# Kernel tuning notes

Hardware: AMD Instinct MI355X
Metric: run time of the kernel (lower is better)

The kernel has to match this reference:

```python
import jax, jax.numpy as jnp
import numpy as np

B = 32
M = 3
MAG_DIM = 20
STD = 0.28
INV = float(1.0 / (np.sqrt(2.0) * STD))
NORM = float(1.0 / (np.sqrt(2.0 * np.pi) * STD))


def _lrelu(x):
    return jax.nn.leaky_relu(x, 0.01)


def _conv(x, w, b):
    y = jax.lax.conv_general_dilated(x, w, (2, 2), 'VALID',
                                     dimension_numbers=('NCHW', 'OIHW', 'NCHW'))
    return _lrelu(y + b[None, :, None, None])


def _combos(x):
    # x: [N, c, d] -> [N, c, c, 2d], pairs[n, i, j] = concat(x[n, i], x[n, j])
    # (matches torch getCombinations: tensorB = expand-over-i, tensorA = expand-over-j)
    N, c, d = x.shape
    left = jnp.broadcast_to(x[:, :, None, :], (N, c, c, d))
    right = jnp.broadcast_to(x[:, None, :, :], (N, c, c, d))
    return jnp.concatenate([left, right], axis=-1)


def _forward(batch, conv_w1, conv_b1, conv_w2, conv_b2, conv_w3, conv_b3, conv_w4, conv_b4,
             post_w, post_b, g_w1, g_b1, g_w2, g_b2, g_w3, g_b3, g_w4, g_b4,
             h_w1, h_b1, h_w2, h_b2, h_w3, h_b3, f_w1, f_b1, f_w2, f_b2, ff_w, ff_b):
    bsz = batch.shape[0]
    x = batch.reshape(bsz * 16, 1, 80, 80)
    # magnitude encoding (computed under no_grad in the original)
    mag = jnp.linspace(-1.0, 1.0, MAG_DIM).astype(batch.dtype)  # [20]
    t = jnp.tanh(x * (2.0 / 255.0) - 1.0)                        # [N,1,80,80]
    enc = NORM * jnp.exp(-(((t + mag[None, :, None, None]) * INV) ** 2))  # [N,20,80,80]
    enc = jax.lax.stop_gradient(enc)
    y = _conv(enc, conv_w1, conv_b1)   # [N,32,39,39]
    y = _conv(y, conv_w2, conv_b2)     # [N,32,19,19]
    y = _conv(y, conv_w3, conv_b3)     # [N,32,9,9]
    y = _conv(y, conv_w4, conv_b4)     # [N,32,4,4]
    obj = y.reshape(bsz * 16, 512) @ post_w + post_b             # [N,247]
    panel = obj.reshape(bsz, 16, 247)
    given, options = panel[:, :8], panel[:, 8:]
    giv = jnp.broadcast_to(given[:, None], (bsz, 8, 8, 247))
    ctx = jnp.concatenate([giv, options[:, :, None, :]], axis=2)  # [B,8,9,247]
    tags = jnp.broadcast_to(jnp.eye(9, dtype=batch.dtype), (bsz * 8, 9, 9))
    objects = jnp.concatenate([ctx.reshape(bsz * 8, 9, 247), tags], axis=-1)  # [B*8,9,256]

    z = _combos(objects).reshape(-1, 512)  # [B*8*81, 512]
    z = _lrelu(z @ g_w1 + g_b1)
    z = _lrelu(z @ g_w2 + g_b2)
    z = _lrelu(z @ g_w3 + g_b3)
    z = _lrelu(z @ g_w4 + g_b4)
    sum_j = z.reshape(bsz * 8, 9, 9, 256).sum(axis=2)  # [B*8,9,256]
    for i in range(h_w1.shape[0]):
        p = _combos(sum_j).reshape(-1, 512)
        z = _lrelu(p @ h_w1[i] + h_b1[i])
        z = _lrelu(z @ h_w2[i] + h_b2[i])
        z = _lrelu(z @ h_w3[i] + h_b3[i])
        sum_j = z.reshape(bsz * 8, 9, 9, 256).sum(axis=2)
    h_sum = sum_j.sum(axis=1)                          # [B*8,256]
    z = _lrelu(h_sum @ f_w1 + f_b1)
    z = _lrelu(z @ f_w2 + f_b2)
    result = z @ ff_w + ff_b                           # [B*8,1]
    answer = result.reshape(bsz, 8)
    loss = jnp.mean(h_sum ** 2) + jnp.mean(result ** 2)
    return answer, loss


def setup_inputs():
    key = jax.random.key(0)
    ks = iter(jax.random.split(key, 40))

    def U(shape, fan_in):
        s = 1.0 / np.sqrt(fan_in)
        return jax.random.uniform(next(ks), shape, jnp.float32, -s, s)

    inp = {
        'batch': jax.random.uniform(next(ks), (B, 16, 80, 80), jnp.float32, 0.0, 255.0),
        'conv_w1': U((32, MAG_DIM, 3, 3), MAG_DIM * 9), 'conv_b1': U((32,), MAG_DIM * 9),
        'conv_w2': U((32, 32, 3, 3), 288), 'conv_b2': U((32,), 288),
        'conv_w3': U((32, 32, 3, 3), 288), 'conv_b3': U((32,), 288),
        'conv_w4': U((32, 32, 3, 3), 288), 'conv_b4': U((32,), 288),
        'post_w': U((512, 247), 512), 'post_b': U((247,), 512),
        'g_w1': U((512, 512), 512), 'g_b1': U((512,), 512),
        'g_w2': U((512, 512), 512), 'g_b2': U((512,), 512),
        'g_w3': U((512, 512), 512), 'g_b3': U((512,), 512),
        'g_w4': U((512, 256), 512), 'g_b4': U((256,), 512),
        'h_w1': U((M, 512, 256), 512), 'h_b1': U((M, 256), 512),
        'h_w2': U((M, 256, 256), 256), 'h_b2': U((M, 256), 256),
        'h_w3': U((M, 256, 256), 256), 'h_b3': U((M, 256), 256),
        'f_w1': U((256, 256), 256), 'f_b1': U((256,), 256),
        'f_w2': U((256, 256), 256), 'f_b2': U((256,), 256),
        'ff_w': U((256, 1), 256), 'ff_b': U((1,), 256),
    }
    return inp


def reference(batch, conv_w1, conv_b1, conv_w2, conv_b2, conv_w3, conv_b3, conv_w4, conv_b4,
              post_w, post_b, g_w1, g_b1, g_w2, g_b2, g_w3, g_b3, g_w4, g_b4,
              h_w1, h_b1, h_w2, h_b2, h_w3, h_b3, f_w1, f_b1, f_w2, f_b2, ff_w, ff_b):
    return _forward(batch, conv_w1, conv_b1, conv_w2, conv_b2, conv_w3, conv_b3, conv_w4, conv_b4,
                    post_w, post_b, g_w1, g_b1, g_w2, g_b2, g_w3, g_b3, g_w4, g_b4,
                    h_w1, h_b1, h_w2, h_b2, h_w3, h_b3, f_w1, f_b1, f_w2, f_b2, ff_w, ff_b)
```

## Files before the change

### kernel.cpp

```cpp
#include <hip/hip_runtime.h>
#include <hip/hip_bf16.h>
#include <math.h>

static __device__ __forceinline__ float lrelu(float v){ return v > 0.0f ? v : 0.01f*v; }

static __device__ __forceinline__ unsigned short f2bf(float f){
  unsigned int u = __float_as_uint(f);
  unsigned int r = (u + 0x7fffu + ((u >> 16) & 1u)) >> 16;
  return (unsigned short)r;
}
static __device__ __forceinline__ float bf2f(unsigned short u){
  return __uint_as_float(((unsigned int)u) << 16);
}
static __device__ __forceinline__ unsigned int pack_bf2(float lo, float hi){
  __hip_bfloat162 bb = __float22bfloat162_rn(make_float2(lo, hi));
  return *reinterpret_cast<unsigned int*>(&bb);
}

#define ENC_NORM 1.4247939f
#define GC_C     6.3775511f
#define GC_2CD   1.3426423f
#define GC_CD2   0.070665395f
#define GC_S1    0.86820227f

typedef __attribute__((ext_vector_type(4))) float f32x4;
typedef __attribute__((ext_vector_type(8))) short bf16x8;

__global__ __launch_bounds__(256) void k_prep(
    const float* __restrict__ g_w1, const float* __restrict__ g_w2,
    const float* __restrict__ g_w3, const float* __restrict__ g_w4,
    const float* __restrict__ h_w1, const float* __restrict__ h_w2,
    const float* __restrict__ h_w3, const float* __restrict__ post_w,
    const float* __restrict__ conv_w2, const float* __restrict__ conv_w3,
    const float* __restrict__ conv_w4, const float* __restrict__ conv_w1,
    const float* __restrict__ f_w1, const float* __restrict__ f_w2,
    unsigned short* __restrict__ WT)
{
  int e = blockIdx.x*256 + threadIdx.x;
  float v;
  if (e < 262144) {
    int nn = e >> 8, kk = e & 255;
    v = (nn < 512) ? g_w1[kk*512 + nn] : g_w1[(256+kk)*512 + (nn-512)];
  } else if (e < 524288) {
    int r = e - 262144; int nn = r >> 9, kk = r & 511;
    v = g_w2[kk*512 + nn];
  } else if (e < 786432) {
    int r = e - 524288; int nn = r >> 9, kk = r & 511;
    v = g_w3[kk*512 + nn];
  } else if (e < 917504) {
    int r = e - 786432; int nn = r >> 9, kk = r & 511;
    v = g_w4[kk*256 + nn];
  } else if (e < 1310720) {
    int r = e - 917504; int i = r >> 17; int q = r & 131071;
    int nn = q >> 8, kk = q & 255;
    v = (nn < 256) ? h_w1[i*131072 + kk*256 + nn]
                   : h_w1[i*131072 + (256+kk)*256 + (nn-256)];
  } else if (e < 1507328) {
    int r = e - 1310720; int i = r >> 16; int q = r & 65535;
    int nn = q >> 8, kk = q & 255;
    v = h_w2[i*65536 + kk*256 + nn];
  } else if (e < 1703936) {
    int r = e - 1507328; int i = r >> 16; int q = r & 65535;
    int nn = q >> 8, kk = q & 255;
    v = h_w3[i*65536 + kk*256 + nn];
  } else if (e < 1835008) {
    int r = e - 1703936; int np = r >> 9, kp = r & 511;
    int px = kp >> 5, c = kp & 31;
    v = (np < 247) ? post_w[(c*16+px)*247 + np] : 0.f;
  } else if (e < 1862656) {
    int r = e - 1835008; int which = r / 9216; int q = r % 9216;
    int tap = q >> 10, o = (q >> 5) & 31, c = q & 31;
    const float* w = which==0 ? conv_w2 : (which==1 ? conv_w3 : conv_w4);
    v = w[(o*32+c)*9 + tap];
  } else if (e < 1871872) {
    int r = e - 1862656; int tap = r >> 10, o = (r >> 5) & 31, c = r & 31;
    v = (c < 20) ? conv_w1[(o*20+c)*9 + tap] : 0.f;
  } else if (e < 1937408) {
    int r = e - 1871872; int nn = r >> 8, kk = r & 255;
    v = f_w1[kk*256 + nn];
  } else {
    int r = e - 1937408; int nn = r >> 8, kk = r & 255;
    v = f_w2[kk*256 + nn];
  }
  WT[e] = f2bf(v);
}

__global__ __launch_bounds__(256) void k_conv1m(
    const float* __restrict__ batch, const unsigned short* __restrict__ wc1,
    const float* __restrict__ bias, unsigned short* __restrict__ y)
{
  __shared__ unsigned short ench[7][80][40];
  int n = blockIdx.x;
  int orow0 = blockIdx.y * 3;
  int irow0 = orow0 * 2;
  int tid = threadIdx.x;
  int lane = tid & 63, wid = tid >> 6;
  int lr = lane & 15, kg = lane >> 4;

  bf16x8 bf0[9], bf1[9];
  #pragma unroll
  for (int tap = 0; tap < 9; ++tap) {
    bf0[tap] = *(const bf16x8*)&wc1[tap*1024 + lr*32 + kg*8];
    bf1[tap] = *(const bf16x8*)&wc1[tap*1024 + (16+lr)*32 + kg*8];
  }

  const float* img = batch + (size_t)n*6400 + irow0*80;
  const float S2 = GC_S1 * GC_S1;
  for (int p = tid; p < 7*79; p += 256) {
    int row = p / 79, col = p % 79;
    float x = img[row*80 + col];
    float E = __expf(x * (4.0f/255.0f) - 2.0f);
    float t = 1.0f - 2.0f*__builtin_amdgcn_rcpf(E + 1.0f);
    float z = t - 1.0f;
    float e = ENC_NORM * __expf(-GC_C*z*z);
    float rg = __expf(-GC_2CD*z - GC_CD2);
    unsigned int pk[16];
    #pragma unroll
    for (int cp = 0; cp < 10; ++cp) {
      float e1 = e * rg;
      pk[cp] = pack_bf2(e, e1);
      e  = e1 * rg * GC_S1;
      rg = rg * S2;
    }
    #pragma unroll
    for (int cp = 10; cp < 16; ++cp) pk[cp] = 0u;
    int hidx = (col & 1) ? 40 + (col >> 1) : (col >> 1);
    unsigned short* dst = &ench[row][hidx][0];
    *(uint4*)(dst)      = *(uint4*)&pk[0];
    *(uint4*)(dst + 8)  = *(uint4*)&pk[4];
    *(uint4*)(dst + 16) = *(uint4*)&pk[8];
    *(uint4*)(dst + 24) = *(uint4*)&pk[12];
  }
  __syncthreads();

  const int totpx = 117;
  float b0 = bias[lr], b1 = bias[16 + lr];
  for (int t = wid; t < 8; t += 4) {
    int pa = t*16 + lr;
    int pc = (pa < totpx) ? pa : (totpx - 1);
    int oh = pc / 39, ow = pc % 39;
    f32x4 acc0 = {0.f,0.f,0.f,0.f}, acc1 = {0.f,0.f,0.f,0.f};
    #pragma unroll
    for (int kh = 0; kh < 3; ++kh) {
      int r = oh*2 + kh;
      #pragma unroll
      for (int kw = 0; kw < 3; ++kw) {
        int hidx = (kw == 1) ? (40 + ow) : (ow + (kw >> 1));
        bf16x8 a = *(const bf16x8*)&ench[r][hidx][kg*8];
        int tap = kh*3 + kw;
        acc0 = __builtin_amdgcn_mfma_f32_16x16x32_bf16(a, bf0[tap], acc0, 0, 0, 0);
        acc1 = __builtin_amdgcn_mfma_f32_16x16x32_bf16(a, bf1[tap], acc1, 0, 0, 0);
      }
    }
    #pragma unroll
    for (int rr = 0; rr < 4; ++rr) {
      int ps = t*16 + kg*4 + rr;
      if (ps < totpx) {
        int soh = orow0 + ps / 39, sow = ps % 39;
        unsigned short* op = y + (((size_t)n*39 + soh)*39 + sow)*32;
        op[lr]      = f2bf(lrelu(acc0[rr] + b0));
        op[16 + lr] = f2bf(lrelu(acc1[rr] + b1));
      }
    }
  }
}

template<int H, int W, int OH, int OW, int ROWS>
__global__ __launch_bounds__(256) void k_cmfma(
    const unsigned short* __restrict__ in, const unsigned short* __restrict__ wc,
    const float* __restrict__ bias, unsigned short* __restrict__ out)
{
  constexpr int IR = 2*ROWS + 1;
  __shared__ unsigned short xs[IR][W][40];
  int n = blockIdx.x;
  int orow0 = blockIdx.y * ROWS;
  int nrows = min(ROWS, OH - orow0);
  int irow0 = orow0 * 2;
  int ir = min(2*nrows + 1, H - irow0);
  int tid = threadIdx.x;
  int lane = tid & 63, wid = tid >> 6;
  int lr = lane & 15, kg = lane >> 4;

  bf16x8 bf0[9], bf1[9];
  #pragma unroll
  for (int tap = 0; tap < 9; ++tap) {
    bf0[tap] = *(const bf16x8*)&wc[(tap*32 + lr)*32      + kg*8];
    bf1[tap] = *(const bf16x8*)&wc[(tap*32 + 16 + lr)*32 + kg*8];
  }

  const unsigned short* ip = in + ((size_t)n*H + irow0)*W*32;
  int npx = ir * W;
  for (int p = tid; p < npx; p += 256) {
    const uint4* src = (const uint4*)(ip + (size_t)p*32);
    uint4 v0 = src[0], v1 = src[1], v2 = src[2], v3 = src[3];
    int r = p / W, col = p % W;
    unsigned short* dst = &xs[r][col][0];
    *(uint4*)(dst)      = v0;
    *(uint4*)(dst + 8)  = v1;
    *(uint4*)(dst + 16) = v2;
    *(uint4*)(dst + 24) = v3;
  }
  __syncthreads();

  int totpx = nrows * OW;
  int ntiles = (totpx + 15) >> 4;
  float b0 = bias[lr], b1 = bias[16 + lr];
  for (int t = wid; t < ntiles; t += 4) {
    int pa = t*16 + lr;
    int pc = (pa < totpx) ? pa : 0;
    int oh = pc / OW, ow = pc % OW;
    f32x4 acc0 = {0.f,0.f,0.f,0.f}, acc1 = {0.f,0.f,0.f,0.f};
    #pragma unroll
    for (int kh = 0; kh < 3; ++kh)
      #pragma unroll
      for (int kw = 0; kw < 3; ++kw) {
        bf16x8 a = *(const bf16x8*)&xs[oh*2 + kh][ow*2 + kw][kg*8];
        acc0 = __builtin_amdgcn_mfma_f32_16x16x32_bf16(a, bf0[kh*3+kw], acc0, 0, 0, 0);
        acc1 = __builtin_amdgcn_mfma_f32_16x16x32_bf16(a, bf1[kh*3+kw], acc1, 0, 0, 0);
      }
    #pragma unroll
    for (int rr = 0; rr < 4; ++rr) {
      int ps = t*16 + kg*4 + rr;
      if (ps < totpx) {
        int soh = orow0 + ps / OW, sow = ps % OW;
        unsigned short* op = out + (((size_t)n*OH + soh)*OW + sow)*32;
        op[lr]      = f2bf(lrelu(acc0[rr] + b0));
        op[16 + lr] = f2bf(lrelu(acc1[rr] + b1));
      }
    }
  }
}

template<int OUT_BF16, int ACT>
__global__ __launch_bounds__(256) void k_mgemm(
    const unsigned short* __restrict__ A, const unsigned short* __restrict__ Wt,
    const float* __restrict__ bias, void* __restrict__ Cv,
    int M, int N, int K)
{
  __shared__ unsigned short As[128][72];
  __shared__ unsigned short Bs[128][72];
  int bm = blockIdx.x * 128;
  int bn = blockIdx.y * 128;
  int tid = threadIdx.x;
  int wid = tid >> 6, lane = tid & 63;
  int wr = (wid >> 1) * 64, wc = (wid & 1) * 64;
  int lr = lane & 15, lk = (lane >> 4) * 8;

  f32x4 acc[4][4];
  #pragma unroll
  for (int i = 0; i < 4; ++i)
    #pragma unroll
    for (int j = 0; j < 4; ++j)
      acc[i][j] = (f32x4){0.f,0.f,0.f,0.f};

  for (int k0 = 0; k0 < K; k0 += 64) {
    #pragma unroll
    for (int i = 0; i < 4; ++i) {
      int ch = tid + (i << 8);
      int r = ch >> 3, kc = (ch & 7) * 8;
      *(uint4*)&As[r][kc] = *(const uint4*)&A[(size_t)(bm + r)*K + k0 + kc];
      *(uint4*)&Bs[r][kc] = *(const uint4*)&Wt[(size_t)(bn + r)*K + k0 + kc];
    }
    __syncthreads();
    #pragma unroll
    for (int ks = 0; ks < 2; ++ks) {
      bf16x8 a[4], b[4];
      #pragma unroll
      for (int i = 0; i < 4; ++i)
        a[i] = *(const bf16x8*)&As[wr + i*16 + lr][ks*32 + lk];
      #pragma unroll
      for (int i = 0; i < 4; ++i)
        b[i] = *(const bf16x8*)&Bs[wc + i*16 + lr][ks*32 + lk];
      #pragma unroll
      for (int i = 0; i < 4; ++i)
        #pragma unroll
        for (int j = 0; j < 4; ++j)
          acc[i][j] = __builtin_amdgcn_mfma_f32_16x16x32_bf16(a[i], b[j], acc[i][j], 0, 0, 0);
    }
    __syncthreads();
  }
  int r0 = (lane >> 4) * 4;
  #pragma unroll
  for (int i = 0; i < 4; ++i) {
    #pragma unroll
    for (int j = 0; j < 4; ++j) {
      int col = bn + wc + j*16 + lr;
      float bv = bias ? bias[col] : 0.f;
      #pragma unroll
      for (int rr = 0; rr < 4; ++rr) {
        int row = bm + wr + i*16 + r0 + rr;
        float v = acc[i][j][rr] + bv;
        if (ACT) v = lrelu(v);
        if (OUT_BF16) ((unsigned short*)Cv)[(size_t)row*N + col] = f2bf(v);
        else          ((float*)Cv)[(size_t)row*N + col] = v;
      }
    }
  }
}

__global__ __launch_bounds__(256) void k_pgemm(
    const unsigned short* __restrict__ UV, const unsigned short* __restrict__ Wt,
    const float* __restrict__ abias, const float* __restrict__ obias,
    unsigned short* __restrict__ C, int M, int N, int K)
{
  __shared__ unsigned short As[128][72];
  __shared__ unsigned short Bs[128][72];
  __shared__ float absm[512];
  int bm = blockIdx.x * 128;
  int bn = blockIdx.y * 128;
  int tid = threadIdx.x;
  int wid = tid >> 6, lane = tid & 63;
  int wr = (wid >> 1) * 64, wc = (wid & 1) * 64;
  int lr = lane & 15, lk = (lane >> 4) * 8;
  int ld = 2*K;

  for (int idx = tid; idx < K; idx += 256) absm[idx] = abias[idx];
  __syncthreads();

  int urow[4], vrow[4];
  #pragma unroll
  for (int i = 0; i < 4; ++i) {
    int r = (tid + (i << 8)) >> 3;
    int m = bm + r;
    int n = m / 81; int rem = m - n*81;
    int ii = rem / 9; int jj = rem - ii*9;
    urow[i] = n*9 + ii; vrow[i] = n*9 + jj;
  }

  f32x4 acc[4][4];
  #pragma unroll
  for (int i = 0; i < 4; ++i)
    #pragma unroll
    for (int j = 0; j < 4; ++j)
      acc[i][j] = (f32x4){0.f,0.f,0.f,0.f};

  for (int k0 = 0; k0 < K; k0 += 64) {
    #pragma unroll
    for (int i = 0; i < 4; ++i) {
      int ch = tid + (i << 8);
      int r = ch >> 3, kc = (ch & 7) * 8;
      uint4 u4 = *(const uint4*)&UV[(size_t)urow[i]*ld + k0 + kc];
      uint4 v4 = *(const uint4*)&UV[(size_t)vrow[i]*ld + K + k0 + kc];
      const unsigned short* us = (const unsigned short*)&u4;
      const unsigned short* vs = (const unsigned short*)&v4;
      unsigned int pk[4];
      #pragma unroll
      for (int e2 = 0; e2 < 4; ++e2) {
        float a0 = bf2f(us[2*e2])   + bf2f(vs[2*e2])   + absm[k0 + kc + 2*e2];
        float a1 = bf2f(us[2*e2+1]) + bf2f(vs[2*e2+1]) + absm[k0 + kc + 2*e2+1];
        pk[e2] = pack_bf2(lrelu(a0), lrelu(a1));
      }
      *(uint4*)&As[r][kc] = *(uint4*)pk;
      *(uint4*)&Bs[r][kc] = *(const uint4*)&Wt[(size_t)(bn + r)*K + k0 + kc];
    }
    __syncthreads();
    #pragma unroll
    for (int ks = 0; ks < 2; ++ks) {
      bf16x8 a[4], b[4];
      #pragma unroll
      for (int i = 0; i < 4; ++i)
        a[i] = *(const bf16x8*)&As[wr + i*16 + lr][ks*32 + lk];
      #pragma unroll
      for (int i = 0; i < 4; ++i)
        b[i] = *(const bf16x8*)&Bs[wc + i*16 + lr][ks*32 + lk];
      #pragma unroll
      for (int i = 0; i < 4; ++i)
        #pragma unroll
        for (int j = 0; j < 4; ++j)
          acc[i][j] = __builtin_amdgcn_mfma_f32_16x16x32_bf16(a[i], b[j], acc[i][j], 0, 0, 0);
    }
    __syncthreads();
  }
  int r0 = (lane >> 4) * 4;
  #pragma unroll
  for (int i = 0; i < 4; ++i) {
    #pragma unroll
    for (int j = 0; j < 4; ++j) {
      int col = bn + wc + j*16 + lr;
      float bv = obias[col];
      #pragma unroll
      for (int rr = 0; rr < 4; ++rr) {
        int row = bm + wr + i*16 + r0 + rr;
        C[(size_t)row*N + col] = f2bf(lrelu(acc[i][j][rr] + bv));
      }
    }
  }
}

__global__ void k_objects(const float* __restrict__ panel, const float* __restrict__ post_b,
                          unsigned short* __restrict__ obj)
{
  int idx = blockIdx.x*256 + threadIdx.x;
  int row = idx >> 8;
  int k = idx & 255;
  int slot = row % 9;
  int nn = row / 9;
  int b = nn >> 3, opt = nn & 7;
  float v;
  if (k < 247) {
    int src = (slot < 8) ? (b*16 + slot) : (b*16 + 8 + opt);
    v = panel[(size_t)src*256 + k] + post_b[k];
  } else {
    v = ((k - 247) == slot) ? 1.0f : 0.0f;
  }
  obj[idx] = f2bf(v);
}

__global__ void k_sumj(const unsigned short* __restrict__ Z, float* __restrict__ SJ,
                       unsigned short* __restrict__ SJb, int C)
{
  int idx = blockIdx.x*256 + threadIdx.x;
  int orow = idx / C, k = idx % C;
  int n = orow / 9, i = orow % 9;
  const unsigned short* base = Z + (size_t)(n*81 + i*9)*C + k;
  float s = 0.f;
  #pragma unroll
  for (int j = 0; j < 9; ++j) s += bf2f(base[(size_t)j*C]);
  SJ[idx] = s;
  SJb[idx] = f2bf(s);
}

__global__ void k_hsum(const float* __restrict__ SJ, float* __restrict__ HS,
                       unsigned short* __restrict__ HSb)
{
  int idx = blockIdx.x*256 + threadIdx.x;
  int n = idx >> 8, k = idx & 255;
  const float* base = SJ + (size_t)n*9*256 + k;
  float s = 0.f;
  #pragma unroll
  for (int i = 0; i < 9; ++i) s += base[i*256];
  HS[idx] = s;
  HSb[idx] = f2bf(s);
}

__global__ __launch_bounds__(256) void k_tailfin(
    const float* __restrict__ HS, const unsigned short* __restrict__ F2,
    const float* __restrict__ ffw, const float* __restrict__ ffb,
    float* __restrict__ out)
{
  __shared__ float red[256];
  __shared__ float wsm[256];
  int tid = threadIdx.x;
  wsm[tid] = ffw[tid];
  float s = 0.f;
  for (int j = 0; j < 256; ++j) { float v = HS[j*256 + tid]; s += v*v; }
  red[tid] = s; __syncthreads();
  for (int off = 128; off > 0; off >>= 1) { if (tid < off) red[tid] += red[tid + off]; __syncthreads(); }
  float hsq = red[0];
  __syncthreads();
  float r = ffb[0];
  for (int k = 0; k < 256; ++k) r += bf2f(F2[(size_t)tid*256 + k])*wsm[k];
  red[tid] = r*r; __syncthreads();
  for (int off = 128; off > 0; off >>= 1) { if (tid < off) red[tid] += red[tid + off]; __syncthreads(); }
  out[tid] = r;
  if (tid == 0) out[256] = hsq/65536.0f + red[0]/256.0f;
}

extern "C" void kernel_launch(void* const* d_in, const int* in_sizes, int n_in,
                              void* d_out, int out_size, void* d_ws, size_t ws_size,
                              hipStream_t stream)
{
  const float* batch   = (const float*)d_in[0];
  const float* conv_w1 = (const float*)d_in[1];
  const float* conv_b1 = (const float*)d_in[2];
  const float* conv_w2 = (const float*)d_in[3];
  const float* conv_b2 = (const float*)d_in[4];
  const float* conv_w3 = (const float*)d_in[5];
  const float* conv_b3 = (const float*)d_in[6];
  const float* conv_w4 = (const float*)d_in[7];
  const float* conv_b4 = (const float*)d_in[8];
  const float* post_w  = (const float*)d_in[9];
  const float* post_b  = (const float*)d_in[10];
  const float* g_w1    = (const float*)d_in[11];
  const float* g_b1    = (const float*)d_in[12];
  const float* g_w2    = (const float*)d_in[13];
  const float* g_b2    = (const float*)d_in[14];
  const float* g_w3    = (const float*)d_in[15];
  const float* g_b3    = (const float*)d_in[16];
  const float* g_w4    = (const float*)d_in[17];
  const float* g_b4    = (const float*)d_in[18];
  const float* h_w1    = (const float*)d_in[19];
  const float* h_b1    = (const float*)d_in[20];
  const float* h_w2    = (const float*)d_in[21];
  const float* h_b2    = (const float*)d_in[22];
  const float* h_w3    = (const float*)d_in[23];
  const float* h_b3    = (const float*)d_in[24];
  const float* f_w1    = (const float*)d_in[25];
  const float* f_b1    = (const float*)d_in[26];
  const float* f_w2    = (const float*)d_in[27];
  const float* f_b2    = (const float*)d_in[28];
  const float* ff_w    = (const float*)d_in[29];
  const float* ff_b    = (const float*)d_in[30];

  char* wsb = (char*)d_ws;
  const size_t off_Y1    = 0;
  const size_t off_Y2    = 52000000;
  const size_t off_Y3    = 64000000;
  const size_t off_Y4    = 67000000;
  const size_t off_PANEL = 68000000;
  const size_t off_WT    = 132000000;
  const size_t off_Pb    = 0;
  const size_t off_Qb    = 22000000;
  const size_t off_UV    = 44000000;
  const size_t off_OBJb  = 54000000;
  const size_t off_SJ    = 56000000;
  const size_t off_SJb   = 59000000;
  const size_t off_HS    = 61000000;
  const size_t off_HSb   = 61500000;
  const size_t off_F1    = 62000000;
  const size_t off_F2    = 63000000;

  unsigned short* WT = (unsigned short*)(wsb + off_WT);
  const size_t wt_g1   = 0;
  const size_t wt_g2   = 262144;
  const size_t wt_g3   = 524288;
  const size_t wt_g4   = 786432;
  const size_t wt_h1   = 917504;
  const size_t wt_h2   = 1310720;
  const size_t wt_h3   = 1507328;
  const size_t wt_post = 1703936;
  const size_t wt_cw2  = 1835008;
  const size_t wt_cw3  = 1844224;
  const size_t wt_cw4  = 1853440;
  const size_t wt_cw1  = 1862656;
  const size_t wt_f1   = 1871872;
  const size_t wt_f2   = 1937408;

  dim3 b256(256);

  k_prep<<<dim3(7824), b256, 0, stream>>>(g_w1, g_w2, g_w3, g_w4, h_w1, h_w2, h_w3,
                                          post_w, conv_w2, conv_w3, conv_w4, conv_w1,
                                          f_w1, f_w2, WT);

  unsigned short* Y1 = (unsigned short*)(wsb + off_Y1);
  unsigned short* Y2 = (unsigned short*)(wsb + off_Y2);
  unsigned short* Y3 = (unsigned short*)(wsb + off_Y3);
  unsigned short* Y4 = (unsigned short*)(wsb + off_Y4);
  float* PANEL = (float*)(wsb + off_PANEL);

  k_conv1m<<<dim3(512,13), b256, 0, stream>>>(batch, WT + wt_cw1, conv_b1, Y1);
  k_cmfma<39,39,19,19,10><<<dim3(512,2), b256, 0, stream>>>(Y1, WT + wt_cw2, conv_b2, Y2);
  k_cmfma<19,19, 9, 9, 9><<<dim3(512,1), b256, 0, stream>>>(Y2, WT + wt_cw3, conv_b3, Y3);
  k_cmfma< 9, 9, 4, 4, 4><<<dim3(512,1), b256, 0, stream>>>(Y3, WT + wt_cw4, conv_b4, Y4);

  k_mgemm<0,0><<<dim3(4,2), b256, 0, stream>>>(Y4, WT + wt_post, nullptr, PANEL, 512,256,512);

  unsigned short* OBJb = (unsigned short*)(wsb + off_OBJb);
  unsigned short* Pb   = (unsigned short*)(wsb + off_Pb);
  unsigned short* Qb   = (unsigned short*)(wsb + off_Qb);
  unsigned short* SJb  = (unsigned short*)(wsb + off_SJb);
  unsigned short* UVb  = (unsigned short*)(wsb + off_UV);
  float* SJ = (float*)(wsb + off_SJ);
  float* HS = (float*)(wsb + off_HS);
  unsigned short* HSb = (unsigned short*)(wsb + off_HSb);
  unsigned short* F1 = (unsigned short*)(wsb + off_F1);
  unsigned short* F2 = (unsigned short*)(wsb + off_F2);

  k_objects<<<dim3(2304), b256, 0, stream>>>(PANEL, post_b, OBJb);

  k_mgemm<1,0><<<dim3(18,8), b256, 0, stream>>>(OBJb, WT + wt_g1, nullptr, UVb, 2304,1024,256);
  k_pgemm<<<dim3(162,4), b256, 0, stream>>>(UVb, WT + wt_g2, g_b1, g_b2, Qb, 20736,512,512);
  k_mgemm<1,1><<<dim3(162,4), b256, 0, stream>>>(Qb, WT + wt_g3, g_b3, Pb, 20736,512,512);
  k_mgemm<1,1><<<dim3(162,2), b256, 0, stream>>>(Pb, WT + wt_g4, g_b4, Qb, 20736,256,512);
  k_sumj<<<dim3(2304), b256, 0, stream>>>(Qb, SJ, SJb, 256);

  for (int i = 0; i < 3; ++i) {
    k_mgemm<1,0><<<dim3(18,4), b256, 0, stream>>>(SJb, WT + wt_h1 + (size_t)i*131072, nullptr, UVb, 2304,512,256);
    k_pgemm<<<dim3(162,2), b256, 0, stream>>>(UVb, WT + wt_h2 + (size_t)i*65536, h_b1 + i*256, h_b2 + i*256, Qb, 20736,256,256);
    k_mgemm<1,1><<<dim3(162,2), b256, 0, stream>>>(Qb, WT + wt_h3 + (size_t)i*65536, h_b3 + i*256, Pb, 20736,256,256);
    k_sumj<<<dim3(2304), b256, 0, stream>>>(Pb, SJ, SJb, 256);
  }

  k_hsum<<<dim3(256), b256, 0, stream>>>(SJ, HS, HSb);
  k_mgemm<1,1><<<dim3(2,2), b256, 0, stream>>>(HSb, WT + wt_f1, f_b1, F1, 256,256,256);
  k_mgemm<1,1><<<dim3(2,2), b256, 0, stream>>>(F1,  WT + wt_f2, f_b2, F2, 256,256,256);
  k_tailfin<<<dim3(1), b256, 0, stream>>>(HS, F2, ff_w, ff_b, (float*)d_out);
}
```

Baseline: 363.5 us.

## Use direct global-to-LDS loads with XOR swizzle and even/odd split conv smem layout

```diff
diff --git a/kernel.cpp b/kernel.cpp
--- a/kernel.cpp
+++ b/kernel.cpp
@@ -15,6 +15,11 @@
 static __device__ __forceinline__ unsigned int pack_bf2(float lo, float hi){
   __hip_bfloat162 bb = __float22bfloat162_rn(make_float2(lo, hi));
   return *reinterpret_cast<unsigned int*>(&bb);
+}
+static __device__ __forceinline__ void gload16(const void* g, void* l){
+  __builtin_amdgcn_global_load_lds(
+    (const __attribute__((address_space(1))) void*)(const void*)g,
+    (__attribute__((address_space(3))) void*)l, 16, 0, 0);
 }
 
 #define ENC_NORM 1.4247939f
@@ -106,8 +111,10 @@
 
   const float* img = batch + (size_t)n*6400 + irow0*80;
   const float S2 = GC_S1 * GC_S1;
-  for (int p = tid; p < 7*79; p += 256) {
-    int row = p / 79, col = p % 79;
+  for (int p = tid; p < 7*80; p += 256) {
+    int row = p / 80, hx = p % 80;
+    int col = (hx < 40) ? 2*hx : 2*(hx-40)+1;
+    if (col > 78) continue;
     float x = img[row*80 + col];
     float E = __expf(x * (4.0f/255.0f) - 2.0f);
     float t = 1.0f - 2.0f*__builtin_amdgcn_rcpf(E + 1.0f);
@@ -124,8 +131,7 @@
     }
     #pragma unroll
     for (int cp = 10; cp < 16; ++cp) pk[cp] = 0u;
-    int hidx = (col & 1) ? 40 + (col >> 1) : (col >> 1);
-    unsigned short* dst = &ench[row][hidx][0];
+    unsigned short* dst = &ench[row][hx][0];
     *(uint4*)(dst)      = *(uint4*)&pk[0];
     *(uint4*)(dst + 8)  = *(uint4*)&pk[4];
     *(uint4*)(dst + 16) = *(uint4*)&pk[8];
@@ -171,6 +177,7 @@
     const float* __restrict__ bias, unsigned short* __restrict__ out)
 {
   constexpr int IR = 2*ROWS + 1;
+  constexpr int EV = (W + 1) / 2;
   __shared__ unsigned short xs[IR][W][40];
   int n = blockIdx.x;
   int orow0 = blockIdx.y * ROWS;
@@ -194,7 +201,8 @@
     const uint4* src = (const uint4*)(ip + (size_t)p*32);
     uint4 v0 = src[0], v1 = src[1], v2 = src[2], v3 = src[3];
     int r = p / W, col = p % W;
-    unsigned short* dst = &xs[r][col][0];
+    int hx = (col & 1) ? EV + (col >> 1) : (col >> 1);
+    unsigned short* dst = &xs[r][hx][0];
     *(uint4*)(dst)      = v0;
     *(uint4*)(dst + 8)  = v1;
     *(uint4*)(dst + 16) = v2;
@@ -214,7 +222,8 @@
     for (int kh = 0; kh < 3; ++kh)
       #pragma unroll
       for (int kw = 0; kw < 3; ++kw) {
-        bf16x8 a = *(const bf16x8*)&xs[oh*2 + kh][ow*2 + kw][kg*8];
+        int hidx = (kw == 1) ? (EV + ow) : (ow + (kw >> 1));
+        bf16x8 a = *(const bf16x8*)&xs[oh*2 + kh][hidx][kg*8];
         acc0 = __builtin_amdgcn_mfma_f32_16x16x32_bf16(a, bf0[kh*3+kw], acc0, 0, 0, 0);
         acc1 = __builtin_amdgcn_mfma_f32_16x16x32_bf16(a, bf1[kh*3+kw], acc1, 0, 0, 0);
       }
@@ -237,14 +246,18 @@
     const float* __restrict__ bias, void* __restrict__ Cv,
     int M, int N, int K)
 {
-  __shared__ unsigned short As[128][72];
-  __shared__ unsigned short Bs[128][72];
+  __shared__ unsigned short As[128*64];
+  __shared__ unsigned short Bs[128*64];
   int bm = blockIdx.x * 128;
   int bn = blockIdx.y * 128;
   int tid = threadIdx.x;
   int wid = tid >> 6, lane = tid & 63;
   int wr = (wid >> 1) * 64, wc = (wid & 1) * 64;
-  int lr = lane & 15, lk = (lane >> 4) * 8;
+  int lr = lane & 15, kg = lane >> 4;
+
+  int srow = lane >> 3;
+  int ssw  = ((lane & 7) * 16) ^ (srow << 4);
+  int rsw  = (lr & 7) << 4;
 
   f32x4 acc[4][4];
   #pragma unroll
@@ -256,21 +269,21 @@
   for (int k0 = 0; k0 < K; k0 += 64) {
     #pragma unroll
     for (int i = 0; i < 4; ++i) {
-      int ch = tid + (i << 8);
-      int r = ch >> 3, kc = (ch & 7) * 8;
-      *(uint4*)&As[r][kc] = *(const uint4*)&A[(size_t)(bm + r)*K + k0 + kc];
-      *(uint4*)&Bs[r][kc] = *(const uint4*)&Wt[(size_t)(bn + r)*K + k0 + kc];
+      int rowc = wid*32 + i*8;
+      int row  = rowc + srow;
+      gload16((const char*)&A[(size_t)(bm + row)*K + k0] + ssw, &As[rowc*64]);
+      gload16((const char*)&Wt[(size_t)(bn + row)*K + k0] + ssw, &Bs[rowc*64]);
     }
     __syncthreads();
     #pragma unroll
     for (int ks = 0; ks < 2; ++ks) {
+      int roff = ((ks*64 + kg*16) ^ rsw) >> 1;
       bf16x8 a[4], b[4];
       #pragma unroll
-      for (int i = 0; i < 4; ++i)
-        a[i] = *(const bf16x8*)&As[wr + i*16 + lr][ks*32 + lk];
-      #pragma unroll
-      for (int i = 0; i < 4; ++i)
-        b[i] = *(const bf16x8*)&Bs[wc + i*16 + lr][ks*32 + lk];
+      for (int i = 0; i < 4; ++i) {
+        a[i] = *(const bf16x8*)&As[(wr + i*16 + lr)*64 + roff];
+        b[i] = *(const bf16x8*)&Bs[(wc + i*16 + lr)*64 + roff];
+      }
       #pragma unroll
       for (int i = 0; i < 4; ++i)
         #pragma unroll
@@ -303,29 +316,36 @@
     const float* __restrict__ abias, const float* __restrict__ obias,
     unsigned short* __restrict__ C, int M, int N, int K)
 {
-  __shared__ unsigned short As[128][72];
-  __shared__ unsigned short Bs[128][72];
+  __shared__ unsigned short As[128*64];
+  __shared__ unsigned short Bs[128*64];
   __shared__ float absm[512];
   int bm = blockIdx.x * 128;
   int bn = blockIdx.y * 128;
   int tid = threadIdx.x;
   int wid = tid >> 6, lane = tid & 63;
   int wr = (wid >> 1) * 64, wc = (wid & 1) * 64;
-  int lr = lane & 15, lk = (lane >> 4) * 8;
+  int lr = lane & 15, kg = lane >> 4;
   int ld = 2*K;
 
+  int srow = lane >> 3;
+  int ssw  = ((lane & 7) * 16) ^ (srow << 4);
+  int rsw  = (lr & 7) << 4;
+
   for (int idx = tid; idx < K; idx += 256) absm[idx] = abias[idx];
-  __syncthreads();
-
-  int urow[4], vrow[4];
+
+  int urow[4], vrow[4], arow[4], asw[4];
   #pragma unroll
   for (int i = 0; i < 4; ++i) {
-    int r = (tid + (i << 8)) >> 3;
+    int ch = tid + (i << 8);
+    int r = ch >> 3;
     int m = bm + r;
     int n = m / 81; int rem = m - n*81;
     int ii = rem / 9; int jj = rem - ii*9;
     urow[i] = n*9 + ii; vrow[i] = n*9 + jj;
-  }
+    arow[i] = r;
+    asw[i] = (((ch & 7) * 16) ^ ((r & 7) << 4)) >> 1;
+  }
+  __syncthreads();
 
   f32x4 acc[4][4];
   #pragma unroll
@@ -337,8 +357,14 @@
   for (int k0 = 0; k0 < K; k0 += 64) {
     #pragma unroll
     for (int i = 0; i < 4; ++i) {
+      int rowc = wid*32 + i*8;
+      int row  = rowc + srow;
+      gload16((const char*)&Wt[(size_t)(bn + row)*K + k0] + ssw, &Bs[rowc*64]);
+    }
+    #pragma unroll
+    for (int i = 0; i < 4; ++i) {
       int ch = tid + (i << 8);
-      int r = ch >> 3, kc = (ch & 7) * 8;
+      int kc = (ch & 7) * 8;
       uint4 u4 = *(const uint4*)&UV[(size_t)urow[i]*ld + k0 + kc];
       uint4 v4 = *(const uint4*)&UV[(size_t)vrow[i]*ld + K + k0 + kc];
       const unsigned short* us = (const unsigned short*)&u4;
@@ -350,19 +376,18 @@
         float a1 = bf2f(us[2*e2+1]) + bf2f(vs[2*e2+1]) + absm[k0 + kc + 2*e2+1];
         pk[e2] = pack_bf2(lrelu(a0), lrelu(a1));
       }
-      *(uint4*)&As[r][kc] = *(uint4*)pk;
-      *(uint4*)&Bs[r][kc] = *(const uint4*)&Wt[(size_t)(bn + r)*K + k0 + kc];
+      *(uint4*)&As[arow[i]*64 + asw[i]] = *(uint4*)pk;
     }
     __syncthreads();
     #pragma unroll
     for (int ks = 0; ks < 2; ++ks) {
+      int roff = ((ks*64 + kg*16) ^ rsw) >> 1;
       bf16x8 a[4], b[4];
       #pragma unroll
-      for (int i = 0; i < 4; ++i)
-        a[i] = *(const bf16x8*)&As[wr + i*16 + lr][ks*32 + lk];
-      #pragma unroll
-      for (int i = 0; i < 4; ++i)
-        b[i] = *(const bf16x8*)&Bs[wc + i*16 + lr][ks*32 + lk];
+      for (int i = 0; i < 4; ++i) {
+        a[i] = *(const bf16x8*)&As[(wr + i*16 + lr)*64 + roff];
+        b[i] = *(const bf16x8*)&Bs[(wc + i*16 + lr)*64 + roff];
+      }
       #pragma unroll
       for (int i = 0; i < 4; ++i)
         #pragma unroll
```

Result: faster. 355.6 us (-2.2%).
